# Performance work log

Hardware: AMD Instinct MI355X
Metric: run time of the kernel (lower is better)

## Reference

```python
import jax, jax.numpy as jnp
import numpy as np

NEG_SLOPE = 0.2  # PyG GATConv default
BN_EPS = 1e-5
NUM_GRAPHS = 128


def _bn(x, g, b, m, v):
    # eval-mode BatchNorm1d with running stats
    return (x - m) * jax.lax.rsqrt(v + BN_EPS) * g + b


def _gat_conv(x, src, dst, mask, W, a_src, a_dst, bias):
    # PyG GATConv: per-head linear, edge logits LeakyReLU(a_src.Wx_j + a_dst.Wx_i),
    # segment-softmax over incoming edges of each dst node, scatter-add messages.
    N = x.shape[0]
    H, C = a_src.shape
    xw = (x @ W).reshape(N, H, C)                       # [N,H,C]
    logit_s = (xw * a_src).sum(-1)                      # [N,H]
    logit_d = (xw * a_dst).sum(-1)                      # [N,H]
    e = jax.nn.leaky_relu(logit_s[src] + logit_d[dst], NEG_SLOPE)  # [E,H]
    e = jnp.where(mask[:, None], e, -1e30)              # edges filtered by edge_weights==1
    m = jax.ops.segment_max(e, dst, num_segments=N)     # [N,H]
    m = jnp.maximum(m, -1e30)                           # guard empty segments
    p = jnp.exp(e - m[dst]) * mask[:, None].astype(e.dtype)
    denom = jax.ops.segment_sum(p, dst, num_segments=N) + 1e-16
    alpha = p / denom[dst]                              # [E,H]
    out = jax.ops.segment_sum(xw[src] * alpha[..., None], dst, num_segments=N)
    return out.reshape(N, H * C) + bias


def setup_inputs() -> dict:
    key = jax.random.key(0)
    ks = jax.random.split(key, 20)
    N, E, F, G, NC = 20000, 320000, 128, NUM_GRAPHS, 10
    E0, E1, H = 256, 512, 2
    C = E1 // H

    def lin(k, fi, fo):
        return jax.random.normal(k, (fi, fo), jnp.float32) / np.float32(np.sqrt(fi))

    def bn(k, n):
        k1, k2, k3, k4 = jax.random.split(k, 4)
        g = 1.0 + 0.1 * jax.random.normal(k1, (n,), jnp.float32)
        b = 0.1 * jax.random.normal(k2, (n,), jnp.float32)
        m = 0.1 * jax.random.normal(k3, (n,), jnp.float32)
        v = 1.0 + 0.5 * jax.random.uniform(k4, (n,), jnp.float32)
        return g, b, m, v

    d = {}
    d['x'] = jax.random.normal(ks[0], (N, F), jnp.float32)
    d['edge_index'] = jax.random.randint(ks[1], (2, E), 0, N, dtype=jnp.int32)
    d['edge_weights'] = jnp.ones((E,), jnp.int32)
    d['batch'] = jnp.sort(jax.random.randint(ks[2], (N,), 0, G, dtype=jnp.int32))
    d['mlp_w1'] = lin(ks[3], F, E0); d['mlp_b1'] = jnp.zeros((E0,), jnp.float32)
    d['bn1_g'], d['bn1_b'], d['bn1_m'], d['bn1_v'] = bn(ks[4], E0)
    d['mlp_w2'] = lin(ks[5], E0, E0); d['mlp_b2'] = jnp.zeros((E0,), jnp.float32)
    d['bn2_g'], d['bn2_b'], d['bn2_m'], d['bn2_v'] = bn(ks[6], E0)
    d['gat0_w'] = lin(ks[7], E0, H * C)
    d['gat0_asrc'] = 0.1 * jax.random.normal(ks[8], (H, C), jnp.float32)
    d['gat0_adst'] = 0.1 * jax.random.normal(ks[9], (H, C), jnp.float32)
    d['gat0_bias'] = jnp.zeros((H * C,), jnp.float32)
    d['gat1_w'] = lin(ks[10], E1, H * C)
    d['gat1_asrc'] = 0.1 * jax.random.normal(ks[11], (H, C), jnp.float32)
    d['gat1_adst'] = 0.1 * jax.random.normal(ks[12], (H, C), jnp.float32)
    d['gat1_bias'] = jnp.zeros((H * C,), jnp.float32)
    d['bn3_g'], d['bn3_b'], d['bn3_m'], d['bn3_v'] = bn(ks[13], E1)
    d['fin_w1'] = lin(ks[14], E1, E1); d['fin_b1'] = jnp.zeros((E1,), jnp.float32)
    d['fin_w2'] = lin(ks[15], E1, NC); d['fin_b2'] = jnp.zeros((NC,), jnp.float32)
    return d


def reference(x, edge_index, edge_weights, batch,
              mlp_w1, mlp_b1, bn1_g, bn1_b, bn1_m, bn1_v,
              mlp_w2, mlp_b2, bn2_g, bn2_b, bn2_m, bn2_v,
              gat0_w, gat0_asrc, gat0_adst, gat0_bias,
              gat1_w, gat1_asrc, gat1_adst, gat1_bias,
              bn3_g, bn3_b, bn3_m, bn3_v,
              fin_w1, fin_b1, fin_w2, fin_b2):
    src, dst = edge_index[0], edge_index[1]
    mask = edge_weights == 1
    # initial MLP (dropout is identity in eval)
    h = jax.nn.relu(_bn(x @ mlp_w1 + mlp_b1, bn1_g, bn1_b, bn1_m, bn1_v))
    h = jax.nn.relu(_bn(h @ mlp_w2 + mlp_b2, bn2_g, bn2_b, bn2_m, bn2_v))
    # GAT layers
    h = _gat_conv(h, src, dst, mask, gat0_w, gat0_asrc, gat0_adst, gat0_bias)
    h = _gat_conv(h, src, dst, mask, gat1_w, gat1_asrc, gat1_adst, gat1_bias)
    # global mean pool over graphs
    sums = jax.ops.segment_sum(h, batch, num_segments=NUM_GRAPHS)
    cnt = jax.ops.segment_sum(jnp.ones((h.shape[0], 1), h.dtype), batch, num_segments=NUM_GRAPHS)
    pooled = sums / jnp.maximum(cnt, 1.0)
    # final head: BN -> ReLU -> Linear -> ReLU -> Linear
    z = jax.nn.relu(_bn(pooled, bn3_g, bn3_b, bn3_m, bn3_v))
    z = jax.nn.relu(z @ fin_w1 + fin_b1)
    return z @ fin_w2 + fin_b2
```

## Files before the change

kernel.cpp:

```cpp
#include <hip/hip_runtime.h>

typedef unsigned short u16;

constexpr int NN = 20000;
constexpr int EE = 320000;
constexpr int FD = 128;
constexpr int C0 = 256;
constexpr int C1 = 512;
constexpr int NG = 128;
constexpr int NC = 10;
constexpr int NBLK = (NN + 255) / 256;
constexpr int HB  = 320;
constexpr int EST = HB * 256;
constexpr int PSPL = 16;

constexpr size_t OFF_XB   = 0;
constexpr size_t OFF_H1   = OFF_XB  + (size_t)NN * FD * 2;
constexpr size_t OFF_H2   = OFF_H1  + (size_t)NN * C0 * 2;
constexpr size_t OFF_XW   = OFF_H2  + (size_t)NN * C0 * 2;
constexpr size_t OFF_H34  = OFF_XW  + (size_t)NN * C1 * 2;
constexpr size_t OFF_LS   = OFF_H34 + (size_t)NN * C1 * 2;
constexpr size_t OFF_LD   = OFF_LS  + (size_t)NN * 2 * 4;
constexpr size_t OFF_DEG  = OFF_LD  + (size_t)NN * 2 * 4;
constexpr size_t OFF_OFFS = OFF_DEG + (size_t)NN * 4;
constexpr size_t OFF_CUR  = OFF_OFFS + 80016;
constexpr size_t OFF_CSRC = OFF_CUR + (size_t)NN * 4;
constexpr size_t OFF_GCNT = OFF_CSRC + (size_t)EE * 4;
constexpr size_t OFF_GOFF = OFF_GCNT + 512;
constexpr size_t OFF_PART = OFF_GOFF + 768;
constexpr size_t OFF_PTOT = OFF_PART + 512;
constexpr size_t OFF_Z1   = OFF_PTOT + 256;
constexpr size_t OFF_Z2   = OFF_Z1  + (size_t)NG * C1 * 2;
constexpr size_t OFF_ST   = OFF_Z2  + (size_t)NG * C1 * 2;
constexpr size_t OFF_W1T  = OFF_ST  + 8192;
constexpr size_t OFF_W2T  = OFF_W1T + (size_t)FD * C0 * 2;
constexpr size_t OFF_G0T  = OFF_W2T + (size_t)C0 * C0 * 2;
constexpr size_t OFF_G1T  = OFF_G0T + (size_t)C0 * C1 * 2;
constexpr size_t OFF_AUX  = OFF_G1T + (size_t)C1 * C1 * 2;
constexpr size_t OFF_FLAG = OFF_AUX  + 0;
constexpr size_t OFF_A0S  = OFF_AUX  + 256;
constexpr size_t OFF_A0D  = OFF_AUX  + 1280;
constexpr size_t OFF_A1S  = OFF_AUX  + 2304;
constexpr size_t OFF_A1D  = OFF_AUX  + 3328;
constexpr size_t OFF_GB0  = OFF_AUX  + 4352;
constexpr size_t OFF_GB1  = OFF_AUX  + 6400;
constexpr size_t OFF_FB1  = OFF_AUX  + 8448;
constexpr size_t OFF_FB2  = OFF_AUX  + 10496;
constexpr size_t OFF_PP   = OFF_AUX  + 11008;
constexpr size_t OFF_DENA = OFF_PP + (size_t)NG * PSPL * C1 * 4;
constexpr size_t OFF_PLS  = OFF_DENA + (size_t)NN * 2 * 4;

__device__ inline float bf2f(u16 u) { return __uint_as_float(((unsigned)u) << 16); }
__device__ inline u16 f2bf(float f) {
    unsigned u = __float_as_uint(f);
    unsigned r = u + 0x7fffu + ((u >> 16) & 1u);
    return (u16)(r >> 16);
}
__device__ inline float ldf(const void* p, long i, unsigned f) {
    return f ? ((const float*)p)[i] : bf2f(((const u16*)p)[i]);
}
__device__ inline void unpack8(uint4 r, float* v) {
    v[0] = __uint_as_float(r.x << 16); v[1] = __uint_as_float(r.x & 0xffff0000u);
    v[2] = __uint_as_float(r.y << 16); v[3] = __uint_as_float(r.y & 0xffff0000u);
    v[4] = __uint_as_float(r.z << 16); v[5] = __uint_as_float(r.z & 0xffff0000u);
    v[6] = __uint_as_float(r.w << 16); v[7] = __uint_as_float(r.w & 0xffff0000u);
}

typedef __bf16 bf16x8_t __attribute__((ext_vector_type(8)));
typedef float  f32x4_t  __attribute__((ext_vector_type(4)));

__device__ __forceinline__ void gl_lds16(const u16* g, u16* l) {
    __builtin_amdgcn_global_load_lds((const __attribute__((address_space(1))) void*)g,
                                     (__attribute__((address_space(3))) void*)l, 16, 0, 0);
}

__global__ void detect_dtype(const u16* __restrict__ x, const u16* __restrict__ w,
                             const u16* __restrict__ fw, unsigned* flag) {
    __shared__ int cnt;
    if (threadIdx.x == 0) cnt = 0;
    __syncthreads();
    int c = 0;
    for (int i = threadIdx.x; i < 4096; i += 256) {
        c += (((x[i]  >> 7) & 0xFF) == 0xFF);
        c += (((w[i]  >> 7) & 0xFF) == 0xFF);
        c += (((fw[i] >> 7) & 0xFF) == 0xFF);
    }
    atomicAdd(&cnt, c);
    __syncthreads();
    if (threadIdx.x == 0) *flag = (cnt >= 2) ? 1u : 0u;
}

__global__ void cvt_x(const unsigned* __restrict__ flag, const void* __restrict__ xin,
                      u16* __restrict__ XB, int* __restrict__ deg, int* __restrict__ gcnt) {
    int i = blockIdx.x * 256 + threadIdx.x;
    if (i < NN) deg[i] = 0;
    if (i < NG) gcnt[i] = 0;
    if (*flag) {
        float4 v = ((const float4*)xin)[i];
        ushort4 r;
        r.x = f2bf(v.x); r.y = f2bf(v.y); r.z = f2bf(v.z); r.w = f2bf(v.w);
        ((ushort4*)XB)[i] = r;
    } else {
        ((ushort4*)XB)[i] = ((const ushort4*)xin)[i];
    }
}

__global__ __launch_bounds__(512) void prep_trans(const unsigned* __restrict__ flag,
                            const void* g1, const void* b1, const void* m1, const void* v1, const void* lb1,
                            const void* g2, const void* b2, const void* m2, const void* v2, const void* lb2,
                            const void* g3, const void* b3, const void* m3, const void* v3,
                            const void* a0s, const void* a0d, const void* gb0in,
                            const void* a1s, const void* a1d, const void* gb1in,
                            const void* fb1in, const void* fb2in,
                            float* S1, float* T1, float* S2, float* T2, float* S3, float* T3,
                            u16* A0S, u16* A0D, u16* A1S, u16* A1D,
                            float* GB0, float* GB1, float* FB1, float* FB2,
                            const void* w1, const void* w2, const void* g0w, const void* g1w,
                            u16* w1T, u16* w2T, u16* g0T, u16* g1T) {
    unsigned f = *flag;
    if (blockIdx.x == 0) {
        int c = threadIdx.x;
        if (c < 256) {
            float s = ldf(g1, c, f) / sqrtf(ldf(v1, c, f) + 1e-5f);
            S1[c] = s; T1[c] = s * (ldf(lb1, c, f) - ldf(m1, c, f)) + ldf(b1, c, f);
            float s2 = ldf(g2, c, f) / sqrtf(ldf(v2, c, f) + 1e-5f);
            S2[c] = s2; T2[c] = s2 * (ldf(lb2, c, f) - ldf(m2, c, f)) + ldf(b2, c, f);
        }
        float s3 = ldf(g3, c, f) / sqrtf(ldf(v3, c, f) + 1e-5f);
        S3[c] = s3; T3[c] = ldf(b3, c, f) - ldf(m3, c, f) * s3;
        A0S[c] = f2bf(ldf(a0s, c, f));
        A0D[c] = f2bf(ldf(a0d, c, f));
        A1S[c] = f2bf(ldf(a1s, c, f));
        A1D[c] = f2bf(ldf(a1d, c, f));
        GB0[c] = ldf(gb0in, c, f);
        GB1[c] = ldf(gb1in, c, f);
        FB1[c] = ldf(fb1in, c, f);
        if (c < NC) FB2[c] = ldf(fb2in, c, f);
        return;
    }
    int b = blockIdx.x - 1;
    const void* B; u16* BT; int K, logN, base;
    if (b < 64)       { B = w1;  BT = w1T; K = FD; logN = 8; base = 0; }
    else if (b < 192) { B = w2;  BT = w2T; K = C0; logN = 8; base = 64; }
    else if (b < 448) { B = g0w; BT = g0T; K = C0; logN = 9; base = 192; }
    else              { B = g1w; BT = g1T; K = C1; logN = 9; base = 448; }
    int idx = (b - base) * 512 + threadIdx.x;
    int N = 1 << logN;
    int k = idx >> logN, n = idx & (N - 1);
    u16 v = f ? f2bf(((const float*)B)[idx]) : ((const u16*)B)[idx];
    BT[(size_t)n * K + k] = v;
}

__global__ __launch_bounds__(256) void hist_k(const int* __restrict__ dst, const int* __restrict__ ew,
                                              const int* __restrict__ batch,
                                              int* __restrict__ deg, int* __restrict__ gcnt) {
    int tid = blockIdx.x * 256 + threadIdx.x;
    int lane = threadIdx.x & 63;
#pragma unroll
    for (int j = 0; j < 4; j++) {
        int e = tid + j * EST;
        if (e < EE && ew[e] == 1) atomicAdd(&deg[dst[e]], 1);
    }
    int n = tid;
    if (n < NN) {
        int g = batch[n];
        int pg = __shfl_up(g, 1);
        bool head = (lane == 0) || (pg != g);
        unsigned long long act = __ballot(1);
        unsigned long long hm  = __ballot(head);
        if (head) {
            unsigned long long above = (lane < 63) ? ((hm >> (lane + 1)) << (lane + 1)) : 0ull;
            int limit = 64 - __builtin_clzll(act);
            int nxt = above ? __builtin_ctzll(above) : limit;
            atomicAdd(&gcnt[g], nxt - lane);
        }
    }
}
__global__ __launch_bounds__(256) void scan_blk(const int* __restrict__ deg, int* __restrict__ off,
                                                int* __restrict__ part) {
    __shared__ int tmp[256];
    int tid = threadIdx.x, i = blockIdx.x * 256 + tid;
    int v = (i < NN) ? deg[i] : 0;
    tmp[tid] = v;
    __syncthreads();
#pragma unroll
    for (int s = 1; s < 256; s <<= 1) {
        int a = (tid >= s) ? tmp[tid - s] : 0;
        __syncthreads();
        if (tid >= s) tmp[tid] += a;
        __syncthreads();
    }
    if (i < NN) off[i] = tmp[tid] - v;
    if (tid == 255) part[blockIdx.x] = tmp[255];
}
__global__ __launch_bounds__(128) void scan_small(int* __restrict__ part, int* __restrict__ ptot,
                                                  const int* __restrict__ gcnt, int* __restrict__ goff) {
    __shared__ int tmp[128];
    int tid = threadIdx.x;
    int v = (tid < NBLK) ? part[tid] : 0;
    tmp[tid] = v;
    __syncthreads();
#pragma unroll
    for (int s = 1; s < 128; s <<= 1) {
        int a = (tid >= s) ? tmp[tid - s] : 0;
        __syncthreads();
        if (tid >= s) tmp[tid] += a;
        __syncthreads();
    }
    if (tid < NBLK) part[tid] = tmp[tid] - v;
    if (tid == 127) *ptot = tmp[127];
    __syncthreads();
    int g = gcnt[tid];
    tmp[tid] = g;
    __syncthreads();
#pragma unroll
    for (int s = 1; s < 128; s <<= 1) {
        int a = (tid >= s) ? tmp[tid - s] : 0;
        __syncthreads();
        if (tid >= s) tmp[tid] += a;
        __syncthreads();
    }
    goff[tid] = tmp[tid] - g;
    if (tid == 127) goff[128] = tmp[127];
}
__global__ __launch_bounds__(256) void scan_add(int* __restrict__ off, const int* __restrict__ part,
                                                const int* __restrict__ ptot, int* __restrict__ cursor) {
    int tid = threadIdx.x, i = blockIdx.x * 256 + tid;
    if (i < NN) {
        int o = off[i] + part[blockIdx.x];
        off[i] = o;
        cursor[i] = o;
    }
    if (i == 0) off[NN] = *ptot;
}
__global__ __launch_bounds__(256) void csr_fill(const int* __restrict__ src, const int* __restrict__ dst,
                                                const int* __restrict__ ew,
                                                int* __restrict__ cursor, u16* __restrict__ csrc) {
    int tid = blockIdx.x * 256 + threadIdx.x;
    bool ok[4]; int sv[4]; int p[4];
#pragma unroll
    for (int j = 0; j < 4; j++) {
        int e = tid + j * EST;
        ok[j] = false; sv[j] = 0; p[j] = 0;
        if (e < EE && ew[e] == 1) {
            ok[j] = true;
            sv[j] = src[e];
            p[j] = atomicAdd(&cursor[dst[e]], 1);
        }
    }
#pragma unroll
    for (int j = 0; j < 4; j++) if (ok[j]) csrc[p[j]] = (u16)sv[j];
}

template <int EPI>
__global__ __launch_bounds__(256) void gemm_tile(const u16* __restrict__ A, const u16* __restrict__ BT,
                                                 u16* __restrict__ Cm,
                                                 const float* __restrict__ S, const float* __restrict__ T,
                                                 const u16* __restrict__ asrc, const u16* __restrict__ adst,
                                                 float2* __restrict__ pls,
                                                 int M, int N, int K) {
    __shared__ u16 As[128 * 64];
    __shared__ u16 Bs[128 * 64];
    const int tid  = threadIdx.x;
    const int wave = tid >> 6;
    const int lane = tid & 63;
    const int quad = lane >> 4;
    const int l16  = lane & 15;
    const int wr0  = (wave >> 1) * 64;
    const int wc0  = (wave & 1) * 64;
    const int row0 = blockIdx.x * 128;
    const int col0 = blockIdx.y * 128;

    const int srow = lane >> 3;
    const int sk   = ((lane & 7) ^ srow) * 8;
    const u16* gaP[4]; const u16* gbP[4]; u16* laP[4]; u16* lbP[4];
#pragma unroll
    for (int i = 0; i < 4; i++) {
        int rl = wave * 32 + i * 8 + srow;
        int gr = row0 + rl; if (gr >= M) gr = M - 1;
        gaP[i] = A  + (size_t)gr * K + sk;
        gbP[i] = BT + (size_t)(col0 + rl) * K + sk;
        laP[i] = As + (size_t)rl * 64 + (lane & 7) * 8;
        lbP[i] = Bs + (size_t)rl * 64 + (lane & 7) * 8;
    }

    f32x4_t acc[4][4];
#pragma unroll
    for (int r = 0; r < 4; r++)
#pragma unroll
        for (int c = 0; c < 4; c++)
#pragma unroll
            for (int i = 0; i < 4; i++) acc[r][c][i] = 0.f;

    for (int k0 = 0; k0 < K; k0 += 64) {
#pragma unroll
        for (int i = 0; i < 4; i++) {
            gl_lds16(gaP[i] + k0, laP[i]);
            gl_lds16(gbP[i] + k0, lbP[i]);
        }
        __syncthreads();

#pragma unroll
        for (int kk = 0; kk < 2; kk++) {
            bf16x8_t a[4], b[4];
#pragma unroll
            for (int r = 0; r < 4; r++) {
                int rr = wr0 + r * 16 + l16;
                a[r] = *(const bf16x8_t*)(As + (size_t)rr * 64 + (((kk * 4 + quad) ^ (rr & 7)) * 8));
            }
#pragma unroll
            for (int c = 0; c < 4; c++) {
                int cc = wc0 + c * 16 + l16;
                b[c] = *(const bf16x8_t*)(Bs + (size_t)cc * 64 + (((kk * 4 + quad) ^ (cc & 7)) * 8));
            }
#pragma unroll
            for (int r = 0; r < 4; r++)
#pragma unroll
                for (int c = 0; c < 4; c++)
                    acc[r][c] = __builtin_amdgcn_mfma_f32_16x16x32_bf16(a[r], b[c], acc[r][c], 0, 0, 0);
        }
        __syncthreads();
    }

    float2* lred = reinterpret_cast<float2*>(As);
#pragma unroll
    for (int r = 0; r < 4; r++) {
        int rb = row0 + wr0 + r * 16 + quad * 4;
        float ps[4] = {0.f, 0.f, 0.f, 0.f}, pd[4] = {0.f, 0.f, 0.f, 0.f};
#pragma unroll
        for (int c = 0; c < 4; c++) {
            int col = col0 + wc0 + c * 16 + l16;
            float sc = (EPI == 1) ? S[col] : 0.f;
            float sh = (EPI == 1) ? T[col] : 0.f;
            float av_ = 0.f, dv_ = 0.f;
            if (EPI == 3) { av_ = bf2f(asrc[col]); dv_ = bf2f(adst[col]); }
#pragma unroll
            for (int i = 0; i < 4; i++) {
                int row = rb + i;
                float v = acc[r][c][i];
                if (EPI == 1) v = fmaxf(v * sc + sh, 0.f);
                u16 bv = f2bf(v);
                if (row < M) Cm[(size_t)row * N + col] = bv;
                if (EPI == 3) {
                    float vb = bf2f(bv);
                    ps[i] = fmaf(vb, av_, ps[i]);
                    pd[i] = fmaf(vb, dv_, pd[i]);
                }
            }
        }
        if (EPI == 3) {
#pragma unroll
            for (int i = 0; i < 4; i++) {
#pragma unroll
                for (int m = 1; m <= 8; m <<= 1) {
                    ps[i] += __shfl_xor(ps[i], m);
                    pd[i] += __shfl_xor(pd[i], m);
                }
            }
            if (l16 == 0) {
#pragma unroll
                for (int i = 0; i < 4; i++) {
                    int rl = wr0 + r * 16 + quad * 4 + i;
                    lred[(size_t)(wave & 1) * 128 + rl] = make_float2(ps[i], pd[i]);
                }
            }
        }
    }
    if (EPI == 3) {
        __syncthreads();
        if (tid < 128) {
            int row = row0 + tid;
            if (row < M) {
                float2 a0 = lred[tid], a1 = lred[128 + tid];
                pls[(size_t)blockIdx.y * NN + row] = make_float2(a0.x + a1.x, a0.y + a1.y);
            }
        }
    }
}

__global__ __launch_bounds__(256) void ls_combine(const float2* __restrict__ pls,
                                                  float* __restrict__ ls, float* __restrict__ ld) {
    int n = blockIdx.x * 256 + threadIdx.x;
    if (n >= NN) return;
#pragma unroll
    for (int h = 0; h < 2; h++) {
        float2 a = pls[(size_t)(2 * h) * NN + n];
        float2 b = pls[(size_t)(2 * h + 1) * NN + n];
        ls[n * 2 + h] = a.x + b.x;
        ld[n * 2 + h] = a.y + b.y;
    }
}

__device__ __forceinline__ void proc_edge(uint4 c, float w, float* acc) {
    float x[8];
    unpack8(c, x);
#pragma unroll
    for (int q = 0; q < 8; q++) acc[q] = fmaf(w, x[q], acc[q]);
}

template <int HALF>
__global__ __launch_bounds__(256) void gat_agg_fused(const int* __restrict__ off, const u16* __restrict__ csrc,
                                                     const float* __restrict__ ls, const float* __restrict__ ld,
                                                     const u16* __restrict__ xw,
                                                     const float* __restrict__ bias, u16* __restrict__ outh) {
    int n = HALF * (NN / 2) + blockIdx.x * 4 + (threadIdx.x >> 6);
    const int lane = threadIdx.x & 63;
    const int h    = lane >> 5;
    const int el   = lane & 31;
    const int hoff = h << 5;
    int beg = off[n], end = off[n + 1];
    float2 ldv = ((const float2*)ld)[n];
    float ldh = h ? ldv.y : ldv.x;

    float vmax = -1e30f;
    for (int base = beg; base < end; base += 32) {
        int e = base + el;
        int ec = e < end ? e : end - 1;
        int sv = csrc[ec];
        float vv = ls[sv * 2 + h] + ldh;
        vv = vv > 0.f ? vv : 0.2f * vv;
        if (e < end) vmax = fmaxf(vmax, vv);
    }
#pragma unroll
    for (int m = 16; m >= 1; m >>= 1) vmax = fmaxf(vmax, __shfl_xor(vmax, m));
    const float mhat = vmax;

    float den = 0.f;
    for (int base = beg; base < end; base += 32) {
        int e = base + el;
        int ec = e < end ? e : end - 1;
        int sv = csrc[ec];
        float vv = ls[sv * 2 + h] + ldh;
        vv = vv > 0.f ? vv : 0.2f * vv;
        float p = __expf(vv - mhat);
        float pm = (e < end) ? p : 0.f;
#pragma unroll
        for (int m = 16; m >= 1; m >>= 1) pm += __shfl_xor(pm, m);
        den += pm;
    }

    float acc[8];
#pragma unroll
    for (int q = 0; q < 8; q++) acc[q] = 0.f;

#define ROWLD(S) (((const uint4*)(xw + (size_t)(S) * C1))[lane])

    for (int base = beg; base < end; base += 32) {
        int cnt = end - base; if (cnt > 32) cnt = 32;
        int e = base + el;
        int ec = e < end ? e : end - 1;
        int sv = csrc[ec];
        float vv = ls[sv * 2 + h] + ldh;
        vv = vv > 0.f ? vv : 0.2f * vv;
        float myp = __expf(vv - mhat);

        uint4 r0 = ROWLD(__shfl(sv, 0));
        uint4 r1 = ROWLD(__shfl(sv, 1));
        uint4 r2 = ROWLD(__shfl(sv, 2));
        uint4 r3 = ROWLD(__shfl(sv, 3));

        for (int j = 0; j < cnt; j += 4) {
            uint4 c0 = r0, c1 = r1, c2 = r2, c3 = r3;
            float w0 = __shfl(myp, j + hoff);
            float w1 = __shfl(myp, j + 1 + hoff);
            float w2 = __shfl(myp, j + 2 + hoff);
            float w3 = __shfl(myp, j + 3 + hoff);
            if (j + 4 < cnt) {
                r0 = ROWLD(__shfl(sv, j + 4));
                r1 = ROWLD(__shfl(sv, j + 5));
                r2 = ROWLD(__shfl(sv, j + 6));
                r3 = ROWLD(__shfl(sv, j + 7));
            }
            proc_edge(c0, w0, acc);
            if (j + 1 < cnt) proc_edge(c1, w1, acc);
            if (j + 2 < cnt) proc_edge(c2, w2, acc);
            if (j + 3 < cnt) proc_edge(c3, w3, acc);
        }
    }
#undef ROWLD

    float inv = 1.f / fmaxf(den, 1e-30f);
    int cb = lane * 8;
    const float4* bp = (const float4*)(bias + cb);
    float4 b0 = bp[0], b1 = bp[1];
    uint4 st;
    st.x = (unsigned)f2bf(fmaf(acc[0], inv, b0.x)) | ((unsigned)f2bf(fmaf(acc[1], inv, b0.y)) << 16);
    st.y = (unsigned)f2bf(fmaf(acc[2], inv, b0.z)) | ((unsigned)f2bf(fmaf(acc[3], inv, b0.w)) << 16);
    st.z = (unsigned)f2bf(fmaf(acc[4], inv, b1.x)) | ((unsigned)f2bf(fmaf(acc[5], inv, b1.y)) << 16);
    st.w = (unsigned)f2bf(fmaf(acc[6], inv, b1.z)) | ((unsigned)f2bf(fmaf(acc[7], inv, b1.w)) << 16);
    ((uint4*)(outh + (size_t)n * C1 + cb))[0] = st;
}

__global__ __launch_bounds__(128) void pool_part(const u16* __restrict__ h4, const int* __restrict__ goff,
                                                 float* __restrict__ pp) {
    int g = blockIdx.x, s = blockIdx.y, t = threadIdx.x;
    int b = goff[g], e = goff[g + 1];
    int len = e - b;
    int chunk = (len + PSPL - 1) / PSPL;
    int n0 = b + s * chunk;
    int n1 = n0 + chunk; if (n1 > e) n1 = e;
    float s0 = 0.f, s1 = 0.f, s2 = 0.f, s3 = 0.f;
    for (int n = n0; n < n1; n++) {
        ushort4 v = *(const ushort4*)(h4 + (size_t)n * C1 + t * 4);
        s0 += bf2f(v.x); s1 += bf2f(v.y); s2 += bf2f(v.z); s3 += bf2f(v.w);
    }
    float4* dst = (float4*)(pp + ((size_t)g * PSPL + s) * C1 + t * 4);
    *dst = make_float4(s0, s1, s2, s3);
}

__global__ __launch_bounds__(512) void head_all(const unsigned* __restrict__ flag,
                                                const float* __restrict__ pp, const int* __restrict__ goff,
                                                const float* __restrict__ S3, const float* __restrict__ T3,
                                                const void* __restrict__ w1, const float* __restrict__ FB1,
                                                const void* __restrict__ w2, const float* __restrict__ FB2,
                                                void* __restrict__ out) {
    __shared__ float zrow[512];
    __shared__ float z2row[512];
    __shared__ float red[512];
    int g = blockIdx.x, t = threadIdx.x;
    unsigned f = *flag;
    float s = 0.f;
#pragma unroll
    for (int k = 0; k < PSPL; k++) s += pp[((size_t)g * PSPL + k) * C1 + t];
    int b = goff[g], e = goff[g + 1];
    float mean = s / fmaxf((float)(e - b), 1.f);
    float v = fmaxf(mean * S3[t] + T3[t], 0.f);
    zrow[t] = bf2f(f2bf(v));
    __syncthreads();
    float acc = 0.f;
    if (f) {
        const float* w = (const float*)w1;
        for (int k = 0; k < 512; k++) acc = fmaf(zrow[k], w[(size_t)k * 512 + t], acc);
    } else {
        const u16* w = (const u16*)w1;
        for (int k = 0; k < 512; k++) acc = fmaf(zrow[k], bf2f(w[(size_t)k * 512 + t]), acc);
    }
    acc += FB1[t];
    z2row[t] = bf2f(f2bf(fmaxf(acc, 0.f)));
    __syncthreads();
    float z2t = z2row[t];
    for (int o = 0; o < NC; o++) {
        float p = f ? z2t * ((const float*)w2)[(size_t)t * NC + o]
                    : z2t * bf2f(((const u16*)w2)[(size_t)t * NC + o]);
        red[t] = p;
        __syncthreads();
#pragma unroll
        for (int sd = 256; sd >= 1; sd >>= 1) {
            if (t < sd) red[t] += red[t + sd];
            __syncthreads();
        }
        if (t == 0) {
            float vv = red[0] + FB2[o];
            if (f) ((float*)out)[g * NC + o] = vv;
            else   ((u16*)out)[g * NC + o] = f2bf(vv);
        }
        __syncthreads();
    }
}

extern "C" void kernel_launch(void* const* d_in, const int* in_sizes, int n_in,
                              void* d_out, int out_size, void* d_ws, size_t ws_size,
                              hipStream_t stream) {
    (void)in_sizes; (void)n_in; (void)out_size; (void)ws_size;

    const void* x      = d_in[0];
    const int* ei      = (const int*)d_in[1];
    const int* src     = ei;
    const int* dst     = ei + EE;
    const int* ew      = (const int*)d_in[2];
    const int* batch   = (const int*)d_in[3];
    const void* mlp_w1 = d_in[4];
    const void* mlp_b1 = d_in[5];
    const void *bn1g = d_in[6], *bn1b = d_in[7], *bn1m = d_in[8], *bn1v = d_in[9];
    const void* mlp_w2 = d_in[10];
    const void* mlp_b2 = d_in[11];
    const void *bn2g = d_in[12], *bn2b = d_in[13], *bn2m = d_in[14], *bn2v = d_in[15];
    const void* g0w    = d_in[16];
    const void* g0as   = d_in[17];
    const void* g0ad   = d_in[18];
    const void* g0bias = d_in[19];
    const void* g1w    = d_in[20];
    const void* g1as   = d_in[21];
    const void* g1ad   = d_in[22];
    const void* g1bias = d_in[23];
    const void *bn3g = d_in[24], *bn3b = d_in[25], *bn3m = d_in[26], *bn3v = d_in[27];
    const void* fin_w1 = d_in[28];
    const void* fin_b1 = d_in[29];
    const void* fin_w2 = d_in[30];
    const void* fin_b2 = d_in[31];

    char* ws = (char*)d_ws;
    u16*  XB   = (u16*)(ws + OFF_XB);
    u16*  h1   = (u16*)(ws + OFF_H1);
    u16*  h2   = (u16*)(ws + OFF_H2);
    u16*  xw   = (u16*)(ws + OFF_XW);
    u16*  h34  = (u16*)(ws + OFF_H34);
    float* ls  = (float*)(ws + OFF_LS);
    float* ld  = (float*)(ws + OFF_LD);
    int*  deg  = (int*)(ws + OFF_DEG);
    int*  off  = (int*)(ws + OFF_OFFS);
    int*  cur  = (int*)(ws + OFF_CUR);
    u16*  csrc = (u16*)(ws + OFF_CSRC);
    int*  gcnt = (int*)(ws + OFF_GCNT);
    int*  goff = (int*)(ws + OFF_GOFF);
    int*  part = (int*)(ws + OFF_PART);
    int*  ptot = (int*)(ws + OFF_PTOT);
    float* S1 = (float*)(ws + OFF_ST);
    float* T1 = S1 + 256;
    float* S2 = T1 + 256;
    float* T2 = S2 + 256;
    float* S3 = T2 + 256;
    float* T3 = S3 + 512;
    u16* w1T = (u16*)(ws + OFF_W1T);
    u16* w2T = (u16*)(ws + OFF_W2T);
    u16* g0T = (u16*)(ws + OFF_G0T);
    u16* g1T = (u16*)(ws + OFF_G1T);
    unsigned* flag = (unsigned*)(ws + OFF_FLAG);
    u16* A0S = (u16*)(ws + OFF_A0S);
    u16* A0D = (u16*)(ws + OFF_A0D);
    u16* A1S = (u16*)(ws + OFF_A1S);
    u16* A1D = (u16*)(ws + OFF_A1D);
    float* GB0 = (float*)(ws + OFF_GB0);
    float* GB1 = (float*)(ws + OFF_GB1);
    float* FB1 = (float*)(ws + OFF_FB1);
    float* FB2 = (float*)(ws + OFF_FB2);
    float* PP = (float*)(ws + OFF_PP);
    float2* PLS = (float2*)(ws + OFF_PLS);

    detect_dtype<<<1, 256, 0, stream>>>((const u16*)x, (const u16*)mlp_w1, (const u16*)fin_w1, flag);
    cvt_x<<<(NN * FD / 4) / 256, 256, 0, stream>>>(flag, x, XB, deg, gcnt);
    prep_trans<<<961, 512, 0, stream>>>(flag,
                                        bn1g, bn1b, bn1m, bn1v, mlp_b1,
                                        bn2g, bn2b, bn2m, bn2v, mlp_b2,
                                        bn3g, bn3b, bn3m, bn3v,
                                        g0as, g0ad, g0bias, g1as, g1ad, g1bias,
                                        fin_b1, fin_b2,
                                        S1, T1, S2, T2, S3, T3,
                                        A0S, A0D, A1S, A1D, GB0, GB1, FB1, FB2,
                                        mlp_w1, mlp_w2, g0w, g1w, w1T, w2T, g0T, g1T);

    hist_k<<<HB, 256, 0, stream>>>(dst, ew, batch, deg, gcnt);
    scan_blk<<<NBLK, 256, 0, stream>>>(deg, off, part);
    scan_small<<<1, 128, 0, stream>>>(part, ptot, gcnt, goff);
    scan_add<<<NBLK, 256, 0, stream>>>(off, part, ptot, cur);
    csr_fill<<<HB, 256, 0, stream>>>(src, dst, ew, cur, csrc);

    gemm_tile<1><<<dim3(157, 2), 256, 0, stream>>>(XB, w1T, h1, S1, T1, nullptr, nullptr, nullptr, NN, C0, FD);
    gemm_tile<1><<<dim3(157, 2), 256, 0, stream>>>(h1, w2T, h2, S2, T2, nullptr, nullptr, nullptr, NN, C0, C0);

    gemm_tile<3><<<dim3(157, 4), 256, 0, stream>>>(h2, g0T, xw, nullptr, nullptr, A0S, A0D, PLS, NN, C1, C0);
    ls_combine<<<NBLK, 256, 0, stream>>>(PLS, ls, ld);
    gat_agg_fused<0><<<(NN / 2) / 4, 256, 0, stream>>>(off, csrc, ls, ld, xw, GB0, h34);
    gat_agg_fused<1><<<(NN / 2) / 4, 256, 0, stream>>>(off, csrc, ls, ld, xw, GB0, h34);

    gemm_tile<3><<<dim3(157, 4), 256, 0, stream>>>(h34, g1T, xw, nullptr, nullptr, A1S, A1D, PLS, NN, C1, C1);
    ls_combine<<<NBLK, 256, 0, stream>>>(PLS, ls, ld);
    gat_agg_fused<0><<<(NN / 2) / 4, 256, 0, stream>>>(off, csrc, ls, ld, xw, GB1, h34);
    gat_agg_fused<1><<<(NN / 2) / 4, 256, 0, stream>>>(off, csrc, ls, ld, xw, GB1, h34);

    pool_part<<<dim3(NG, PSPL), 128, 0, stream>>>(h34, goff, PP);
    head_all<<<NG, 512, 0, stream>>>(flag, PP, goff, S3, T3, fin_w1, FB1, fin_w2, FB2, d_out);
}
```

Baseline: 377.6 us.

## Use LDS-tiled weight transpose and online softmax in GAT aggregation

The weight transpose in prep_trans now goes through a 64x64 shared-memory tile, so global reads and writes are both coalesced instead of writes being strided by K. The grid shrinks to 121 blocks of 256 threads. The GAT aggregation kernel merges its separate max pass and denominator pass into a single online-softmax pass with running max rescaling, removing one gather sweep over neighbour logits per node. This costs an extra exp per chunk plus a cross-lane max reduction inside the loop.

```diff
diff --git a/kernel.cpp b/kernel.cpp
--- a/kernel.cpp
+++ b/kernel.cpp
@@ -105,7 +105,7 @@
     }
 }
 
-__global__ __launch_bounds__(512) void prep_trans(const unsigned* __restrict__ flag,
+__global__ __launch_bounds__(256) void prep_trans(const unsigned* __restrict__ flag,
                             const void* g1, const void* b1, const void* m1, const void* v1, const void* lb1,
                             const void* g2, const void* b2, const void* m2, const void* v2, const void* lb2,
                             const void* g3, const void* b3, const void* m3, const void* v3,
@@ -119,36 +119,51 @@
                             u16* w1T, u16* w2T, u16* g0T, u16* g1T) {
     unsigned f = *flag;
     if (blockIdx.x == 0) {
-        int c = threadIdx.x;
-        if (c < 256) {
-            float s = ldf(g1, c, f) / sqrtf(ldf(v1, c, f) + 1e-5f);
-            S1[c] = s; T1[c] = s * (ldf(lb1, c, f) - ldf(m1, c, f)) + ldf(b1, c, f);
-            float s2 = ldf(g2, c, f) / sqrtf(ldf(v2, c, f) + 1e-5f);
-            S2[c] = s2; T2[c] = s2 * (ldf(lb2, c, f) - ldf(m2, c, f)) + ldf(b2, c, f);
-        }
-        float s3 = ldf(g3, c, f) / sqrtf(ldf(v3, c, f) + 1e-5f);
-        S3[c] = s3; T3[c] = ldf(b3, c, f) - ldf(m3, c, f) * s3;
-        A0S[c] = f2bf(ldf(a0s, c, f));
-        A0D[c] = f2bf(ldf(a0d, c, f));
-        A1S[c] = f2bf(ldf(a1s, c, f));
-        A1D[c] = f2bf(ldf(a1d, c, f));
-        GB0[c] = ldf(gb0in, c, f);
-        GB1[c] = ldf(gb1in, c, f);
-        FB1[c] = ldf(fb1in, c, f);
-        if (c < NC) FB2[c] = ldf(fb2in, c, f);
+        for (int c = threadIdx.x; c < 512; c += 256) {
+            if (c < 256) {
+                float s = ldf(g1, c, f) / sqrtf(ldf(v1, c, f) + 1e-5f);
+                S1[c] = s; T1[c] = s * (ldf(lb1, c, f) - ldf(m1, c, f)) + ldf(b1, c, f);
+                float s2 = ldf(g2, c, f) / sqrtf(ldf(v2, c, f) + 1e-5f);
+                S2[c] = s2; T2[c] = s2 * (ldf(lb2, c, f) - ldf(m2, c, f)) + ldf(b2, c, f);
+            }
+            float s3 = ldf(g3, c, f) / sqrtf(ldf(v3, c, f) + 1e-5f);
+            S3[c] = s3; T3[c] = ldf(b3, c, f) - ldf(m3, c, f) * s3;
+            A0S[c] = f2bf(ldf(a0s, c, f));
+            A0D[c] = f2bf(ldf(a0d, c, f));
+            A1S[c] = f2bf(ldf(a1s, c, f));
+            A1D[c] = f2bf(ldf(a1d, c, f));
+            GB0[c] = ldf(gb0in, c, f);
+            GB1[c] = ldf(gb1in, c, f);
+            FB1[c] = ldf(fb1in, c, f);
+            if (c < NC) FB2[c] = ldf(fb2in, c, f);
+        }
         return;
     }
+    __shared__ u16 tile[64][65];
     int b = blockIdx.x - 1;
-    const void* B; u16* BT; int K, logN, base;
-    if (b < 64)       { B = w1;  BT = w1T; K = FD; logN = 8; base = 0; }
-    else if (b < 192) { B = w2;  BT = w2T; K = C0; logN = 8; base = 64; }
-    else if (b < 448) { B = g0w; BT = g0T; K = C0; logN = 9; base = 192; }
-    else              { B = g1w; BT = g1T; K = C1; logN = 9; base = 448; }
-    int idx = (b - base) * 512 + threadIdx.x;
-    int N = 1 << logN;
-    int k = idx >> logN, n = idx & (N - 1);
-    u16 v = f ? f2bf(((const float*)B)[idx]) : ((const u16*)B)[idx];
-    BT[(size_t)n * K + k] = v;
+    const void* B; u16* BT; int K, N, base;
+    if (b < 8)       { B = w1;  BT = w1T; K = FD; N = C0; base = 0;  }
+    else if (b < 24) { B = w2;  BT = w2T; K = C0; N = C0; base = 8;  }
+    else if (b < 56) { B = g0w; BT = g0T; K = C0; N = C1; base = 24; }
+    else             { B = g1w; BT = g1T; K = C1; N = C1; base = 56; }
+    int t = b - base;
+    int ntn = N >> 6;
+    int k0 = (t / ntn) * 64;
+    int n0 = (t % ntn) * 64;
+    int r = threadIdx.x >> 6;
+    int c = threadIdx.x & 63;
+#pragma unroll
+    for (int i = 0; i < 16; i++) {
+        int kk = r * 16 + i;
+        size_t idx = (size_t)(k0 + kk) * N + n0 + c;
+        tile[kk][c] = f ? f2bf(((const float*)B)[idx]) : ((const u16*)B)[idx];
+    }
+    __syncthreads();
+#pragma unroll
+    for (int i = 0; i < 16; i++) {
+        int nn = r * 16 + i;
+        BT[(size_t)(n0 + nn) * K + k0 + c] = tile[c][nn];
+    }
 }
 
 __global__ __launch_bounds__(256) void hist_k(const int* __restrict__ dst, const int* __restrict__ ew,
@@ -412,32 +427,24 @@
     float2 ldv = ((const float2*)ld)[n];
     float ldh = h ? ldv.y : ldv.x;
 
-    float vmax = -1e30f;
+    float m = -1e30f, den = 0.f;
     for (int base = beg; base < end; base += 32) {
         int e = base + el;
         int ec = e < end ? e : end - 1;
         int sv = csrc[ec];
         float vv = ls[sv * 2 + h] + ldh;
         vv = vv > 0.f ? vv : 0.2f * vv;
-        if (e < end) vmax = fmaxf(vmax, vv);
-    }
-#pragma unroll
-    for (int m = 16; m >= 1; m >>= 1) vmax = fmaxf(vmax, __shfl_xor(vmax, m));
-    const float mhat = vmax;
-
-    float den = 0.f;
-    for (int base = beg; base < end; base += 32) {
-        int e = base + el;
-        int ec = e < end ? e : end - 1;
-        int sv = csrc[ec];
-        float vv = ls[sv * 2 + h] + ldh;
-        vv = vv > 0.f ? vv : 0.2f * vv;
-        float p = __expf(vv - mhat);
-        float pm = (e < end) ? p : 0.f;
-#pragma unroll
-        for (int m = 16; m >= 1; m >>= 1) pm += __shfl_xor(pm, m);
-        den += pm;
-    }
+        float vm = (e < end) ? vv : -1e30f;
+#pragma unroll
+        for (int mm = 16; mm >= 1; mm >>= 1) vm = fmaxf(vm, __shfl_xor(vm, mm));
+        float mn = fmaxf(m, vm);
+        float p = (e < end) ? __expf(vv - mn) : 0.f;
+#pragma unroll
+        for (int mm = 16; mm >= 1; mm >>= 1) p += __shfl_xor(p, mm);
+        den = den * __expf(m - mn) + p;
+        m = mn;
+    }
+    const float mhat = m;
 
     float acc[8];
 #pragma unroll
@@ -629,7 +636,7 @@
 
     detect_dtype<<<1, 256, 0, stream>>>((const u16*)x, (const u16*)mlp_w1, (const u16*)fin_w1, flag);
     cvt_x<<<(NN * FD / 4) / 256, 256, 0, stream>>>(flag, x, XB, deg, gcnt);
-    prep_trans<<<961, 512, 0, stream>>>(flag,
+    prep_trans<<<121, 256, 0, stream>>>(flag,
                                         bn1g, bn1b, bn1m, bn1v, mlp_b1,
                                         bn2g, bn2b, bn2m, bn2v, mlp_b2,
                                         bn3g, bn3b, bn3m, bn3v,
```

New measurement: 378.5 us. No clear change (+0.3%).
